# Optimization experiments

Hardware: AMD Instinct MI355X
Metric: run time of the kernel (lower is better)

Reference implementation:

```python
import jax, jax.numpy as jnp
import numpy as np

N_TOKENS, OUT, E, H, D = 32, 1, 768, 12, 8
B, L = 64, 256
DH = E // H


def layer_norm(x, g, b, eps=1e-5):
    mu = jnp.mean(x, axis=-1, keepdims=True)
    var = jnp.mean((x - mu) ** 2, axis=-1, keepdims=True)
    return (x - mu) * jax.lax.rsqrt(var + eps) * g + b


def setup_inputs() -> dict:
    key = jax.random.key(0)
    ks = jax.random.split(key, 16)
    tokens = jax.random.randint(ks[0], (B, L), 0, N_TOKENS)
    padding = jnp.zeros((B, L), dtype=bool)
    r = jax.random.normal(ks[1], (B, L, 3), dtype=jnp.float32) * 3.0
    s = 0.02
    embed = jax.random.normal(ks[2], (N_TOKENS, E), jnp.float32) * s
    embed = embed.at[0].set(0.0)  # padding_idx=0
    inp = dict(
        tokens=tokens, padding=padding, r=r, embed=embed,
        mu=jax.random.uniform(ks[3], (D, H), jnp.float32, 0.0, 4.0),
        gamma=jax.random.uniform(ks[4], (D, H), jnp.float32, 0.1, 1.0),
        w=jax.random.normal(ks[5], (D, H), jnp.float32),
        Wqkv=jax.random.normal(ks[6], (D, E, 3 * E), jnp.float32) * s,
        bqkv=jnp.zeros((D, 3 * E), jnp.float32),
        Wo=jax.random.normal(ks[7], (D, E, E), jnp.float32) * s,
        bo=jnp.zeros((D, E), jnp.float32),
        ln1_g=jnp.ones((D, E), jnp.float32), ln1_b=jnp.zeros((D, E), jnp.float32),
        W1=jax.random.normal(ks[8], (D, E, 4 * E), jnp.float32) * s,
        b1=jnp.zeros((D, 4 * E), jnp.float32),
        W2=jax.random.normal(ks[9], (D, 4 * E, E), jnp.float32) * s,
        b2=jnp.zeros((D, E), jnp.float32),
        ln2_g=jnp.ones((D, E), jnp.float32), ln2_b=jnp.zeros((D, E), jnp.float32),
        lnf_g=jnp.ones((E,), jnp.float32), lnf_b=jnp.zeros((E,), jnp.float32),
        Wout=jax.random.normal(ks[10], (E, OUT), jnp.float32) * s,
        bout=jnp.zeros((OUT,), jnp.float32),
    )
    return inp


def reference(tokens, padding, r, embed, mu, gamma, w, Wqkv, bqkv, Wo, bo,
              ln1_g, ln1_b, W1, b1, W2, b2, ln2_g, ln2_b, lnf_g, lnf_b, Wout, bout):
    Bc, Lc = tokens.shape
    # pairwise distances (eps for grad stability at d=0 on diagonal)
    diff = r[:, :, None, :] - r[:, None, :, :]              # [B,L,L,3]
    d = jnp.sqrt(jnp.sum(diff * diff, axis=-1) + 1e-12)     # [B,L,L]
    diag = jnp.eye(Lc, dtype=bool)
    pad_pair = padding[:, None, :] | padding[:, :, None]    # [B,L,L]
    attn_mask = (pad_pair | diag)[:, None, :, :]            # [B,1,L,L] True=blocked
    pad_e = padding[:, :, None]                              # [B,L,1]
    neg = jnp.asarray(-1e9, jnp.float32)

    e = embed[tokens]                                        # [B,L,E]
    scale = 1.0 / np.sqrt(DH)
    for i in range(D):
        # learned per-head Gaussian RBF attention bias
        bias = w[i][None, :, None, None] * jnp.exp(
            -gamma[i][None, :, None, None] * (d[:, None, :, :] - mu[i][None, :, None, None]) ** 2
        )                                                    # [B,H,L,L]
        e0 = layer_norm(e, ln1_g[i], ln1_b[i])
        qkv = e0 @ Wqkv[i] + bqkv[i]
        q, k, v = jnp.split(qkv, 3, axis=-1)
        q = q.reshape(Bc, Lc, H, DH).transpose(0, 2, 1, 3)
        k = k.reshape(Bc, Lc, H, DH).transpose(0, 2, 1, 3)
        v = v.reshape(Bc, Lc, H, DH).transpose(0, 2, 1, 3)
        scores = jnp.einsum('bhid,bhjd->bhij', q, k) * scale + bias
        scores = jnp.where(attn_mask, neg, scores)
        a = jax.nn.softmax(scores, axis=-1)
        o = jnp.einsum('bhij,bhjd->bhid', a, v)
        o = o.transpose(0, 2, 1, 3).reshape(Bc, Lc, E)
        e1 = o @ Wo[i] + bo[i]
        e2 = layer_norm(e1 + e0, ln2_g[i], ln2_b[i])
        e3 = jax.nn.relu(e2 @ W1[i] + b1[i]) @ W2[i] + b2[i]
        e3 = jnp.where(pad_e, 0.0, e3)
        e = e3 + e2
    e = layer_norm(e, lnf_g, lnf_b)
    e = jnp.mean(e, axis=1)
    return e @ Wout + bout
```

## Files before the change

### kernel.cpp

```cpp
#include <hip/hip_runtime.h>
#include <cstdint>
#include <cstddef>

#define B_    64
#define L_    256
#define E_    768
#define H_    12
#define DH_   64
#define D_    8
#define FF_   3072
#define QKV3_ 2304
#define M_    (B_*L_)

typedef _Float16 f16;
typedef f16   f16x8  __attribute__((ext_vector_type(8)));
typedef float f32x4  __attribute__((ext_vector_type(4)));

__device__ __forceinline__ void gl_lds16(const void* g, void* l){
    __builtin_amdgcn_global_load_lds(
        (const __attribute__((address_space(1))) void*)g,
        (__attribute__((address_space(3))) void*)l, 16, 0, 0);
}

__global__ void sentinel_kernel(float* out, int n){
    int i = blockIdx.x*64 + threadIdx.x;
    if (i < n) out[i] = 1.0e6f;
}

__global__ __launch_bounds__(256) void gather_kernel(
    const int* __restrict__ tok, const float* __restrict__ emb, float* __restrict__ e)
{
    const int idx = blockIdx.x*256 + threadIdx.x;
    const int row = idx / E_;
    const int d   = idx - row*E_;
    e[idx] = emb[(size_t)tok[row]*E_ + d];
}

__global__ void wsplit_kernel(const float* __restrict__ W, f16* __restrict__ Hh, int K, int N)
{
    __shared__ float tile[32][33];
    const int tx = threadIdx.x, ty = threadIdx.y;
#pragma unroll
    for (int i2 = 0; i2 < 4; ++i2){
        const int k = blockIdx.y*32 + ty + i2*8;
        const int n = blockIdx.x*32 + tx;
        tile[ty + i2*8][tx] = W[(size_t)k*N + n];
    }
    __syncthreads();
    const int k2 = blockIdx.y*32 + tx;
#pragma unroll
    for (int i2 = 0; i2 < 4; ++i2){
        const int n2 = blockIdx.x*32 + ty + i2*8;
        Hh[(size_t)n2*K + k2] = (f16)tile[tx][ty + i2*8];
    }
}

__global__ __launch_bounds__(256) void ln_kernel(
    const float* __restrict__ x, const float* __restrict__ g, const float* __restrict__ bb,
    float* __restrict__ yF, f16* __restrict__ yH, f16* __restrict__ yL)
{
    __shared__ float red[256];
    const int row = blockIdx.x, tid = threadIdx.x;
    const float* xr = x + (size_t)row*E_;
    float v0 = xr[tid], v1 = xr[tid+256], v2 = xr[tid+512];
    red[tid] = v0 + v1 + v2;
    __syncthreads();
    for (int o = 128; o; o >>= 1){ if (tid < o) red[tid] += red[tid+o]; __syncthreads(); }
    const float mean = red[0] * (1.f/768.f);
    __syncthreads();
    const float d0 = v0-mean, d1 = v1-mean, d2 = v2-mean;
    red[tid] = d0*d0 + d1*d1 + d2*d2;
    __syncthreads();
    for (int o = 128; o; o >>= 1){ if (tid < o) red[tid] += red[tid+o]; __syncthreads(); }
    const float rstd = rsqrtf(red[0]*(1.f/768.f) + 1e-5f);
    const float dv[3] = {d0, d1, d2};
#pragma unroll
    for (int q = 0; q < 3; ++q){
        const int d = tid + q*256;
        const float y = dv[q]*rstd*g[d] + bb[d];
        const size_t idx = (size_t)row*E_ + d;
        if (yF) yF[idx] = y;
        if (yH){
            const f16 hi = (f16)y;
            yH[idx] = hi;
            yL[idx] = (f16)(y - (float)hi);
        }
    }
}

template<int MODE>
__global__ __launch_bounds__(256, 4) void gemm_kernel(
    const f16* __restrict__ A, const f16* __restrict__ Bh,
    const float* __restrict__ bias,
    const f16* __restrict__ exH, const f16* __restrict__ exL,
    const unsigned char* __restrict__ pad,
    float* __restrict__ Cf, f16* __restrict__ Cq,
    f16* __restrict__ qh, f16* __restrict__ kh, f16* __restrict__ vt,
    int Mn, int Nn, int Kn)
{
    __shared__ f16 sA[128*32];
    __shared__ f16 sB[128*32];
    const int tid = threadIdx.x;
    const int w = tid >> 6, l = tid & 63;
    const int nt = gridDim.x;
    const int flat = blockIdx.y * nt + blockIdx.x;
    const int xcd = flat & 7, grp = flat >> 3;
    const int bx = grp % nt;
    const int by = xcd + 8 * (grp / nt);
    const int m0 = by * 128, n0 = bx * 128;
    const int waveM = (w & 1) * 64, waveN = (w >> 1) * 64;
    const int fr = l & 15, fq = l >> 4;
    f32x4 acc[4][4] = {};

    const int e0i = tid * 8;
    const int r0  = e0i >> 5, k0o = e0i & 31;
    const int e1i = e0i + 2048;
    const int r1  = e1i >> 5, k1o = e1i & 31;

    for (int kk = 0; kk < Kn; kk += 32){
        __syncthreads();
        {
            const size_t a0 = (size_t)(m0 + r0) * Kn + kk + k0o;
            const size_t a1 = (size_t)(m0 + r1) * Kn + kk + k1o;
            const size_t b0 = (size_t)(n0 + r0) * Kn + kk + k0o;
            const size_t b1 = (size_t)(n0 + r1) * Kn + kk + k1o;
            gl_lds16(A  + a0, &sA[e0i]);
            gl_lds16(A  + a1, &sA[e1i]);
            gl_lds16(Bh + b0, &sB[e0i]);
            gl_lds16(Bh + b1, &sB[e1i]);
        }
        __syncthreads();
        f16x8 fa[4], fb[4];
#pragma unroll
        for (int i = 0; i < 4; ++i){
            fa[i] = *(const f16x8*)&sA[(waveM + i*16 + fr)*32 + fq*8];
            fb[i] = *(const f16x8*)&sB[(waveN + i*16 + fr)*32 + fq*8];
        }
#pragma unroll
        for (int i = 0; i < 4; ++i)
#pragma unroll
            for (int j = 0; j < 4; ++j)
                acc[i][j] = __builtin_amdgcn_mfma_f32_16x16x32_f16(fa[i], fb[j], acc[i][j], 0,0,0);
    }
#pragma unroll
    for (int jt = 0; jt < 4; ++jt){
        const int col = n0 + waveN + jt*16 + fr;
        const float bc = bias[col];
        int which = 0, hh = 0, dd = 0;
        if (MODE == 0){
            which = col / 768;
            const int hc = col - which*768;
            hh = hc >> 6; dd = hc & 63;
        }
#pragma unroll
        for (int it = 0; it < 4; ++it)
#pragma unroll
            for (int rg = 0; rg < 4; ++rg){
                const int row = m0 + waveM + it*16 + fq*4 + rg;
                float v = acc[it][jt][rg] + bc;
                if (MODE == 0){
                    const int bb2 = row >> 8, jj2 = row & 255;
                    const size_t bh = (size_t)bb2 * H_ + hh;
                    if (which == 0)      qh[(bh*256 + jj2)*64 + dd] = (f16)v;
                    else if (which == 1) kh[(bh*256 + jj2)*64 + dd] = (f16)v;
                    else                 vt[(bh*64 + dd)*256 + jj2] = (f16)v;
                } else {
                    const size_t idx = (size_t)row * Nn + col;
                    if (MODE == 1){
                        Cf[idx] = v + (float)exH[idx] + (float)exL[idx];
                    } else if (MODE == 2){
                        Cq[idx] = (f16)fmaxf(v, 0.f);
                    } else {
                        if (pad[row]) v = 0.f;
                        Cf[idx] = v + (float)exH[idx] + (float)exL[idx];
                    }
                }
            }
    }
}

__global__ __launch_bounds__(256, 4) void attn_kernel(
    const f16* __restrict__ qh, const f16* __restrict__ kh, const f16* __restrict__ vt,
    const float* __restrict__ rpos, const unsigned char* __restrict__ pad,
    const float* __restrict__ mu, const float* __restrict__ ga, const float* __restrict__ wv,
    f16* __restrict__ o)
{
    __shared__ f16 sK[64*72];
    __shared__ f16 sV[64*72];
    __shared__ f16 sP[4][16*72];
    __shared__ float rx[256], ry[256], rz[256], pf[256];

    const int h = blockIdx.x, b = blockIdx.y, p = blockIdx.z;
    const int tid = threadIdx.x, w = tid >> 6, l = tid & 63;
    const int fr = l & 15, fq = l >> 4;
    const float muh = mu[h], gah = ga[h], wh = wv[h];
    const size_t bh = (size_t)b * H_ + h;
    const int rowbase = b * L_;

    rx[tid] = rpos[(size_t)(rowbase+tid)*3 + 0];
    ry[tid] = rpos[(size_t)(rowbase+tid)*3 + 1];
    rz[tid] = rpos[(size_t)(rowbase+tid)*3 + 2];
    pf[tid] = pad[rowbase+tid] ? 1.f : 0.f;

    f16x8 fQ[2];
    {
        const int r = p*64 + w*16 + fr;
        const f16* qp = qh + (bh*256 + r)*64 + fq*8;
        fQ[0] = *(const f16x8*)(qp);
        fQ[1] = *(const f16x8*)(qp + 32);
    }

    float m_[4], l_[4];
    f32x4 oacc[4] = {};
#pragma unroll
    for (int rg = 0; rg < 4; ++rg){ m_[rg] = -3.0e38f; l_[rg] = 0.f; }
    __syncthreads();

    for (int c = 0; c < 4; ++c){
        __syncthreads();
        {
            const int e0 = tid*8, e1 = e0 + 2048;
            const int kr0 = e0 >> 6, kd0 = e0 & 63;
            const int kr1 = e1 >> 6, kd1 = e1 & 63;
            *(uint4*)&sK[kr0*72 + kd0] = *(const uint4*)&kh[(bh*256 + c*64 + kr0)*64 + kd0];
            *(uint4*)&sK[kr1*72 + kd1] = *(const uint4*)&kh[(bh*256 + c*64 + kr1)*64 + kd1];
            *(uint4*)&sV[kr0*72 + kd0] = *(const uint4*)&vt[(bh*64 + kr0)*256 + c*64 + kd0];
            *(uint4*)&sV[kr1*72 + kd1] = *(const uint4*)&vt[(bh*64 + kr1)*256 + c*64 + kd1];
        }
        __syncthreads();
        f32x4 sacc[4] = {};
#pragma unroll
        for (int nt = 0; nt < 4; ++nt)
#pragma unroll
            for (int kf = 0; kf < 2; ++kf){
                const f16x8 fb = *(const f16x8*)&sK[(nt*16 + fr)*72 + kf*32 + fq*8];
                sacc[nt] = __builtin_amdgcn_mfma_f32_16x16x32_f16(fQ[kf], fb, sacc[nt], 0,0,0);
            }
        float sv[4][4];
        float rmax[4] = {-3.0e38f, -3.0e38f, -3.0e38f, -3.0e38f};
        const int ibase = p*64 + w*16 + fq*4;
#pragma unroll
        for (int nt = 0; nt < 4; ++nt){
            const int j = c*64 + nt*16 + fr;
            const float jx = rx[j], jy = ry[j], jz = rz[j], jp = pf[j];
#pragma unroll
            for (int rg = 0; rg < 4; ++rg){
                const int i = ibase + rg;
                const float dx = rx[i]-jx, dy = ry[i]-jy, dz = rz[i]-jz;
                const float dist = sqrtf(dx*dx + dy*dy + dz*dz + 1e-12f);
                const float t = dist - muh;
                float s = sacc[nt][rg]*0.125f + wh*__expf(-gah*t*t);
                if ((j == i) | (pf[i] != 0.f) | (jp != 0.f)) s = -1e9f;
                sv[nt][rg] = s;
                rmax[rg] = fmaxf(rmax[rg], s);
            }
        }
#pragma unroll
        for (int rg = 0; rg < 4; ++rg){
#pragma unroll
            for (int off = 8; off >= 1; off >>= 1)
                rmax[rg] = fmaxf(rmax[rg], __shfl_xor(rmax[rg], off));
            const float mnew = fmaxf(m_[rg], rmax[rg]);
            const float alpha = __expf(m_[rg] - mnew);
            m_[rg] = mnew;
            l_[rg] *= alpha;
#pragma unroll
            for (int dt = 0; dt < 4; ++dt) oacc[dt][rg] *= alpha;
            float rs = 0.f;
#pragma unroll
            for (int nt = 0; nt < 4; ++nt){
                const float pv = __expf(sv[nt][rg] - mnew);
                sP[w][(fq*4 + rg)*72 + nt*16 + fr] = (f16)pv;
                rs += pv;
            }
#pragma unroll
            for (int off = 8; off >= 1; off >>= 1) rs += __shfl_xor(rs, off);
            l_[rg] += rs;
        }
#pragma unroll
        for (int kf = 0; kf < 2; ++kf){
            const f16x8 pa = *(const f16x8*)&sP[w][fr*72 + kf*32 + fq*8];
#pragma unroll
            for (int dt = 0; dt < 4; ++dt){
                const f16x8 vb = *(const f16x8*)&sV[(dt*16 + fr)*72 + kf*32 + fq*8];
                oacc[dt] = __builtin_amdgcn_mfma_f32_16x16x32_f16(pa, vb, oacc[dt], 0,0,0);
            }
        }
    }
    const int rglob = rowbase + p*64 + w*16 + fq*4;
#pragma unroll
    for (int rg = 0; rg < 4; ++rg){
        const float inv = 1.f / l_[rg];
#pragma unroll
        for (int dt = 0; dt < 4; ++dt)
            o[(size_t)(rglob + rg)*E_ + h*64 + dt*16 + fr] = (f16)(oacc[dt][rg]*inv);
    }
}

__global__ __launch_bounds__(256) void mean_kernel(const float* __restrict__ x, float* __restrict__ m)
{
    const int b = blockIdx.x, tid = threadIdx.x;
    const float* xb = x + (size_t)b*L_*E_;
#pragma unroll
    for (int q = 0; q < 3; ++q){
        const int d = tid + q*256;
        float s = 0.f;
        for (int l2 = 0; l2 < L_; ++l2) s += xb[(size_t)l2*E_ + d];
        m[b*E_ + d] = s * (1.f/(float)L_);
    }
}

__global__ __launch_bounds__(256) void out_kernel(
    const float* __restrict__ m, const float* __restrict__ Wout,
    const float* __restrict__ bout, float* __restrict__ out)
{
    __shared__ float red[256];
    const int b = blockIdx.x, tid = threadIdx.x;
    float s = 0.f;
#pragma unroll
    for (int q = 0; q < 3; ++q){ const int d = tid + q*256; s += m[b*E_ + d]*Wout[d]; }
    red[tid] = s;
    __syncthreads();
    for (int o = 128; o; o >>= 1){ if (tid < o) red[tid] += red[tid+o]; __syncthreads(); }
    if (tid == 0) out[b] = red[0] + bout[0];
}

extern "C" void kernel_launch(void* const* d_in, const int* in_sizes, int n_in,
                              void* d_out, int out_size, void* d_ws, size_t ws_size,
                              hipStream_t stream)
{
    const int*            tokens  = (const int*)d_in[0];
    const unsigned char*  padding = (const unsigned char*)d_in[1];
    const float*          rpos    = (const float*)d_in[2];
    const float*          embed   = (const float*)d_in[3];
    const float*          mu      = (const float*)d_in[4];
    const float*          ga      = (const float*)d_in[5];
    const float*          wv      = (const float*)d_in[6];
    const float*          Wqkv    = (const float*)d_in[7];
    const float*          bqkv    = (const float*)d_in[8];
    const float*          Wo      = (const float*)d_in[9];
    const float*          bo      = (const float*)d_in[10];
    const float*          ln1g    = (const float*)d_in[11];
    const float*          ln1b    = (const float*)d_in[12];
    const float*          W1      = (const float*)d_in[13];
    const float*          b1      = (const float*)d_in[14];
    const float*          W2      = (const float*)d_in[15];
    const float*          b2      = (const float*)d_in[16];
    const float*          ln2g    = (const float*)d_in[17];
    const float*          ln2b    = (const float*)d_in[18];
    const float*          lnfg    = (const float*)d_in[19];
    const float*          lnfb    = (const float*)d_in[20];
    const float*          Wout    = (const float*)d_in[21];
    const float*          bout    = (const float*)d_in[22];
    float* out = (float*)d_out;
    (void)in_sizes; (void)n_in;

    char* ws = (char*)d_ws;
    size_t off = 0;
    auto alloc = [&](size_t bytes)->char*{
        char* p = ws + off;
        off += (bytes + 255) & ~(size_t)255;
        return p;
    };
    const size_t PLANE = (size_t)M_*E_;
    float* e     = (float*)alloc(PLANE*4);
    char*  big   = alloc(PLANE*2*4);
    f16*   actH  = (f16*)alloc(PLANE*2);
    f16*   actL  = (f16*)alloc(PLANE*2);
    f16*   wqh   = (f16*)alloc((size_t)E_*QKV3_*2);
    f16*   woh   = (f16*)alloc((size_t)E_*E_*2);
    f16*   w1h   = (f16*)alloc((size_t)E_*FF_*2);
    f16*   w2h   = (f16*)alloc((size_t)FF_*E_*2);
    float* meanb = (float*)alloc((size_t)B_*E_*4);
    const size_t required = off;

    if (ws_size < required){
        sentinel_kernel<<<dim3((out_size+63)/64), dim3(64), 0, stream>>>(out, out_size);
        return;
    }

    f16*   qh   = (f16*)big;
    f16*   kh   = qh + PLANE;
    f16*   vt   = kh + PLANE;
    f16*   ob   = vt + PLANE;
    f16*   hbuf = (f16*)big;
    float* lnfo = (float*)big;
    float* sbuf = e;

    gather_kernel<<<dim3(M_*E_/256), dim3(256), 0, stream>>>(tokens, embed, e);

    for (int i = 0; i < D_; ++i){
        wsplit_kernel<<<dim3(QKV3_/32, E_/32), dim3(32,8), 0, stream>>>(
            Wqkv + (size_t)i*E_*QKV3_, wqh, E_, QKV3_);
        wsplit_kernel<<<dim3(E_/32, E_/32), dim3(32,8), 0, stream>>>(
            Wo + (size_t)i*E_*E_, woh, E_, E_);
        wsplit_kernel<<<dim3(FF_/32, E_/32), dim3(32,8), 0, stream>>>(
            W1 + (size_t)i*E_*FF_, w1h, E_, FF_);
        wsplit_kernel<<<dim3(E_/32, FF_/32), dim3(32,8), 0, stream>>>(
            W2 + (size_t)i*FF_*E_, w2h, FF_, E_);

        ln_kernel<<<dim3(M_), dim3(256), 0, stream>>>(e, ln1g + i*E_, ln1b + i*E_, nullptr, actH, actL);
        gemm_kernel<0><<<dim3(QKV3_/128, M_/128), dim3(256), 0, stream>>>(
            actH, wqh, bqkv + i*QKV3_, nullptr, nullptr, nullptr,
            nullptr, nullptr, qh, kh, vt, M_, QKV3_, E_);
        attn_kernel<<<dim3(H_, B_, 4), dim3(256), 0, stream>>>(
            qh, kh, vt, rpos, padding, mu + i*H_, ga + i*H_, wv + i*H_, ob);
        gemm_kernel<1><<<dim3(E_/128, M_/128), dim3(256), 0, stream>>>(
            ob, woh, bo + i*E_, actH, actL, nullptr,
            sbuf, nullptr, nullptr, nullptr, nullptr, M_, E_, E_);
        ln_kernel<<<dim3(M_), dim3(256), 0, stream>>>(sbuf, ln2g + i*E_, ln2b + i*E_, nullptr, actH, actL);
        gemm_kernel<2><<<dim3(FF_/128, M_/128), dim3(256), 0, stream>>>(
            actH, w1h, b1 + i*FF_, nullptr, nullptr, nullptr,
            nullptr, hbuf, nullptr, nullptr, nullptr, M_, FF_, E_);
        gemm_kernel<3><<<dim3(E_/128, M_/128), dim3(256), 0, stream>>>(
            hbuf, w2h, b2 + i*E_, actH, actL, padding,
            e, nullptr, nullptr, nullptr, nullptr, M_, E_, FF_);
    }

    ln_kernel<<<dim3(M_), dim3(256), 0, stream>>>(e, lnfg, lnfb, lnfo, nullptr, nullptr);
    mean_kernel<<<dim3(B_), dim3(256), 0, stream>>>(lnfo, meanb);
    out_kernel<<<dim3(B_), dim3(256), 0, stream>>>(meanb, Wout, bout, out);
}
```

Baseline: 4.840 ms.

## Double-buffer LDS tiles in GEMM kernel to overlap loads with MFMA

Splits the shared-memory A/B tiles into two ping-pong buffers. The next K-slice is issued with global_load_lds into one buffer while MFMA runs on the other, cutting the barrier count per K step from two to one. The goal is to hide global-to-LDS latency behind matrix math. LDS use per block doubles, which could reduce occupancy, and the loop assumes an even number of K steps.

After: 4.724 ms. 2.4% less time.

```diff
diff --git a/kernel.cpp b/kernel.cpp
--- a/kernel.cpp
+++ b/kernel.cpp
@@ -98,8 +98,10 @@
     f16* __restrict__ qh, f16* __restrict__ kh, f16* __restrict__ vt,
     int Mn, int Nn, int Kn)
 {
-    __shared__ f16 sA[128*32];
-    __shared__ f16 sB[128*32];
+    __shared__ f16 sA0[128*32];
+    __shared__ f16 sA1[128*32];
+    __shared__ f16 sB0[128*32];
+    __shared__ f16 sB1[128*32];
     const int tid = threadIdx.x;
     const int w = tid >> 6, l = tid & 63;
     const int nt = gridDim.x;
@@ -117,31 +119,47 @@
     const int e1i = e0i + 2048;
     const int r1  = e1i >> 5, k1o = e1i & 31;
 
-    for (int kk = 0; kk < Kn; kk += 32){
+    const f16* pa0 = A  + (size_t)(m0 + r0) * Kn + k0o;
+    const f16* pa1 = A  + (size_t)(m0 + r1) * Kn + k1o;
+    const f16* pb0 = Bh + (size_t)(n0 + r0) * Kn + k0o;
+    const f16* pb1 = Bh + (size_t)(n0 + r1) * Kn + k1o;
+
+#define STAGE_(SA, SB, KK) do { \
+        gl_lds16(pa0 + (KK), &SA[e0i]); \
+        gl_lds16(pa1 + (KK), &SA[e1i]); \
+        gl_lds16(pb0 + (KK), &SB[e0i]); \
+        gl_lds16(pb1 + (KK), &SB[e1i]); \
+    } while(0)
+
+#define COMPUTE_(SA, SB) do { \
+        f16x8 fa[4], fb[4]; \
+        _Pragma("unroll") \
+        for (int i = 0; i < 4; ++i){ \
+            fa[i] = *(const f16x8*)&SA[(waveM + i*16 + fr)*32 + fq*8]; \
+            fb[i] = *(const f16x8*)&SB[(waveN + i*16 + fr)*32 + fq*8]; \
+        } \
+        _Pragma("unroll") \
+        for (int i = 0; i < 4; ++i) \
+        _Pragma("unroll") \
+        for (int j = 0; j < 4; ++j) \
+            acc[i][j] = __builtin_amdgcn_mfma_f32_16x16x32_f16(fa[i], fb[j], acc[i][j], 0,0,0); \
+    } while(0)
+
+    const int nsteps = Kn >> 5;
+    STAGE_(sA0, sB0, 0);
+    __syncthreads();
+    for (int s = 0; s < nsteps; s += 2){
+        STAGE_(sA1, sB1, (s+1)*32);
+        COMPUTE_(sA0, sB0);
         __syncthreads();
-        {
-            const size_t a0 = (size_t)(m0 + r0) * Kn + kk + k0o;
-            const size_t a1 = (size_t)(m0 + r1) * Kn + kk + k1o;
-            const size_t b0 = (size_t)(n0 + r0) * Kn + kk + k0o;
-            const size_t b1 = (size_t)(n0 + r1) * Kn + kk + k1o;
-            gl_lds16(A  + a0, &sA[e0i]);
-            gl_lds16(A  + a1, &sA[e1i]);
-            gl_lds16(Bh + b0, &sB[e0i]);
-            gl_lds16(Bh + b1, &sB[e1i]);
-        }
-        __syncthreads();
-        f16x8 fa[4], fb[4];
-#pragma unroll
-        for (int i = 0; i < 4; ++i){
-            fa[i] = *(const f16x8*)&sA[(waveM + i*16 + fr)*32 + fq*8];
-            fb[i] = *(const f16x8*)&sB[(waveN + i*16 + fr)*32 + fq*8];
-        }
-#pragma unroll
-        for (int i = 0; i < 4; ++i)
-#pragma unroll
-            for (int j = 0; j < 4; ++j)
-                acc[i][j] = __builtin_amdgcn_mfma_f32_16x16x32_f16(fa[i], fb[j], acc[i][j], 0,0,0);
-    }
+        const bool more = (s + 2 < nsteps);
+        if (more) STAGE_(sA0, sB0, (s+2)*32);
+        COMPUTE_(sA1, sB1);
+        if (more) __syncthreads();
+    }
+#undef STAGE_
+#undef COMPUTE_
+
 #pragma unroll
     for (int jt = 0; jt < 4; ++jt){
         const int col = n0 + waveN + jt*16 + fr;
```
